# Optimization experiments

Hardware: AMD Instinct MI355X
Metric: run time of the kernel (lower is better)

Reference implementation:

```python
import jax, jax.numpy as jnp
import numpy as np
import math

B, Hdim, Wdim, C = 8, 64, 64, 512
T, TXT = 77, 512
NH, HD = 8, 64  # num_heads, head_dim
TOP_M = 3
CLAMP_LOGIT = 2.0
CONF_THRESH = 0.35
NEG_INF = -1e30


def _ln(x, g, b, eps=1e-5):
    mu = x.mean(-1, keepdims=True)
    var = ((x - mu) ** 2).mean(-1, keepdims=True)
    return (x - mu) * jax.lax.rsqrt(var + eps) * g + b


def _l2norm(x, eps=1e-6):
    n = jnp.sqrt((x * x).sum(-1, keepdims=True))
    return x / jnp.maximum(n, eps)


def setup_inputs() -> dict:
    key = jax.random.key(0)
    ks = jax.random.split(key, 16)
    s = 0.02
    inp = {
        'visual_features': jax.random.normal(ks[0], (B, Hdim, Wdim, C), jnp.float32),
        'text_features': jax.random.normal(ks[1], (B, T, TXT), jnp.float32),
        'ln1_g': jnp.ones((C,), jnp.float32), 'ln1_b': jnp.zeros((C,), jnp.float32),
        'ln2_g': jnp.ones((C,), jnp.float32), 'ln2_b': jnp.zeros((C,), jnp.float32),
        'Wq': jax.random.normal(ks[2], (C, C), jnp.float32) * s, 'bq': jnp.zeros((C,), jnp.float32),
        'Wk': jax.random.normal(ks[3], (TXT, C), jnp.float32) * s, 'bk': jnp.zeros((C,), jnp.float32),
        'Wv': jax.random.normal(ks[4], (TXT, C), jnp.float32) * s, 'bv': jnp.zeros((C,), jnp.float32),
        'Wo': jax.random.normal(ks[5], (C, C), jnp.float32) * s, 'bo': jnp.zeros((C,), jnp.float32),
        'Wg': jax.random.normal(ks[6], (C, 1), jnp.float32) * s, 'bg': jnp.zeros((1,), jnp.float32),
        'W1': jax.random.normal(ks[7], (C, 4 * C), jnp.float32) * s, 'b1': jnp.zeros((4 * C,), jnp.float32),
        'W2': jax.random.normal(ks[8], (4 * C, C), jnp.float32) * s, 'b2': jnp.zeros((C,), jnp.float32),
        'logit_scale': jnp.asarray(math.log(1.0 / 0.07), jnp.float32),
        'alpha': jnp.asarray(0.1, jnp.float32),
    }
    return inp


def reference(visual_features, text_features, ln1_g, ln1_b, ln2_g, ln2_b,
              Wq, bq, Wk, bk, Wv, bv, Wo, bo, Wg, bg, W1, b1, W2, b2,
              logit_scale, alpha):
    b, h, w, c = visual_features.shape
    n = h * w
    # Pre-LN on visual tokens
    x = _ln(visual_features, ln1_g, ln1_b).reshape(b, n, c)
    q_full = x @ Wq + bq                                   # [B,N,C]
    pad_mask = jnp.abs(text_features).sum(-1) <= 1e-6      # [B,T]
    k_full = text_features @ Wk + bk                       # [B,T,C]
    v_full = text_features @ Wv + bv
    # l2-normalize over full channel dim, then split heads
    q = _l2norm(q_full).reshape(b, n, NH, HD)
    k = _l2norm(k_full).reshape(b, T, NH, HD)
    v = v_full.reshape(b, T, NH, HD)
    scale = jnp.exp(jnp.clip(logit_scale, -CLAMP_LOGIT, CLAMP_LOGIT)) / math.sqrt(float(HD))
    sim = jnp.einsum('bnhd,bthd->bnht', q, k) * scale      # [B,N,H,T]
    sim = jnp.where(pad_mask[:, None, None, :], NEG_INF, sim)
    # top-k sparsification: keep top_m per (b,n,h) row
    topv = jax.lax.top_k(sim, TOP_M)[0][..., -1:]
    sim = jnp.where(sim >= topv, sim, NEG_INF)
    attn = jax.nn.softmax(sim, axis=-1)
    attn = attn / jnp.maximum(attn.sum(-1, keepdims=True), 1e-6)
    all_pad = pad_mask.all(axis=1)                         # [B]
    attn = jnp.where(all_pad[:, None, None, None], 0.0, attn)
    # confidence: max-prob * (1 - normalized entropy), mean over heads
    attn_hn = attn.transpose(0, 2, 1, 3)                   # [B,H,N,T]
    maxp = attn_hn.max(-1, keepdims=True)
    t_eff = jnp.maximum((attn_hn > 0).astype(jnp.float32).sum(-1, keepdims=True), 2.0)
    p = jnp.maximum(attn_hn, 1e-8)
    entropy = jnp.maximum(-(p * jnp.log(p)).sum(-1, keepdims=True) / jnp.log(t_eff), 0.0)
    conf = jnp.clip(maxp * (1.0 - entropy), 0.0, 1.0).mean(axis=1)  # [B,N,1]
    bypass = (conf >= CONF_THRESH).astype(attn.dtype)
    aligned = jnp.einsum('bnht,bthd->bnhd', attn, v).reshape(b, n, c)
    aligned = (aligned @ Wo + bo) * bypass
    gate = jax.nn.sigmoid(x @ Wg + bg)                     # [B,N,1]
    y = x + alpha * gate * aligned
    y = _ln(y, ln2_g, ln2_b)
    y = y + (jax.nn.gelu(y @ W1 + b1, approximate=False) @ W2 + b2)
    return y.reshape(b, h, w, c)
```

## Files before the change

kernel.cpp:

```cpp
#include <hip/hip_runtime.h>
#include <stdint.h>

#define BATCH 8
#define NTOK 4096
#define CDIM 512
#define TTXT 77
#define TPAD 80
#define NHEAD 8
#define HDIM 64
#define HID 2048
#define MROWS 32768
#define NEGINF (-1e30f)

typedef __attribute__((ext_vector_type(8))) short short8;
typedef __attribute__((ext_vector_type(4))) float f32x4;

__device__ __forceinline__ float b2f(unsigned short u) {
    union { unsigned int i; float f; } x; x.i = ((unsigned int)u) << 16; return x.f;
}
__device__ __forceinline__ unsigned short f2b(float f) {
    union { float f; unsigned int i; } x; x.f = f;
    unsigned int i = x.i;
    return (unsigned short)((i + 0x7fffu + ((i >> 16) & 1u)) >> 16);
}

__device__ __forceinline__ void gload16(const void* g, void* l) {
    __builtin_amdgcn_global_load_lds(
        (const __attribute__((address_space(1))) unsigned int*)g,
        (__attribute__((address_space(3))) unsigned int*)l, 16, 0, 0);
}

#define OFF_WQT   ((size_t)0)
#define OFF_WKT   (OFF_WQT + 512*512*2)
#define OFF_WVT   (OFF_WKT + 512*512*2)
#define OFF_WOT   (OFF_WVT + 512*512*2)
#define OFF_W1T   (OFF_WOT + 512*512*2)
#define OFF_W2T   (OFF_W1T + (size_t)2048*512*2)
#define OFF_TEXTB (OFF_W2T + (size_t)512*2048*2)
#define OFF_KFB   (OFF_TEXTB + (size_t)640*512*2)
#define OFF_KNRM  (OFF_KFB + (size_t)640*512*2)
#define OFF_VPAD  (OFF_KNRM + (size_t)640*512*2)
#define OFF_PADM  (OFF_VPAD + (size_t)640*512*2)
#define OFF_ALLP  (OFF_PADM + 2560)
#define OFF_GATE  (OFF_ALLP + 256)
#define OFF_BYP   (OFF_GATE + (size_t)MROWS*4)
#define OFF_XB    (OFF_BYP + (size_t)MROWS*4)
#define OFF_BUFB  (OFF_XB + (size_t)MROWS*CDIM*2)
#define OFF_BUFC  (OFF_BUFB + (size_t)MROWS*CDIM*2)
#define OFF_H     (OFF_BUFC + (size_t)MROWS*CDIM*2)
#define WS_NEED   (OFF_H + (size_t)MROWS*HID*2)
#define OFF_VT    OFF_H

__device__ __forceinline__ float waveReduceAdd(float v) {
#pragma unroll
    for (int m = 1; m < 64; m <<= 1) v += __shfl_xor(v, m);
    return v;
}
__device__ __forceinline__ float waveReduceMin(float v) {
#pragma unroll
    for (int m = 1; m < 64; m <<= 1) v = fminf(v, __shfl_xor(v, m));
    return v;
}
__device__ __forceinline__ float red16Max(float v) {
#pragma unroll
    for (int m = 1; m < 16; m <<= 1) v = fmaxf(v, __shfl_xor(v, m));
    return v;
}
__device__ __forceinline__ float red16Add(float v) {
#pragma unroll
    for (int m = 1; m < 16; m <<= 1) v += __shfl_xor(v, m);
    return v;
}

__global__ __launch_bounds__(256) void transpose_all_kernel(
    const float* __restrict__ Wq, const float* __restrict__ Wk,
    const float* __restrict__ Wv, const float* __restrict__ Wo,
    const float* __restrict__ W1, const float* __restrict__ W2,
    unsigned short* __restrict__ WQT, unsigned short* __restrict__ WKT,
    unsigned short* __restrict__ WVT, unsigned short* __restrict__ WOT,
    unsigned short* __restrict__ W1T, unsigned short* __restrict__ W2T)
{
    __shared__ float tile[32][33];
    int b = blockIdx.x;
    const float* src; unsigned short* dst; int R, C, cx, ry;
    if (b < 1024)       { src = W1; dst = W1T; R = 512;  C = 2048; cx = b & 63; ry = b >> 6; }
    else if (b < 2048)  { b -= 1024; src = W2; dst = W2T; R = 2048; C = 512; cx = b & 15; ry = b >> 4; }
    else {
        b -= 2048; const int which = b >> 8; b &= 255;
        R = 512; C = 512; cx = b & 15; ry = b >> 4;
        src = (which == 0) ? Wq : (which == 1) ? Wk : (which == 2) ? Wv : Wo;
        dst = (which == 0) ? WQT : (which == 1) ? WKT : (which == 2) ? WVT : WOT;
    }
    const int tx = threadIdx.x & 31, ty = threadIdx.x >> 5;
    const int c0 = cx * 32, r0 = ry * 32;
#pragma unroll
    for (int i = 0; i < 32; i += 8)
        tile[ty + i][tx] = src[(size_t)(r0 + ty + i) * C + c0 + tx];
    __syncthreads();
#pragma unroll
    for (int i = 0; i < 32; i += 8)
        dst[(size_t)(c0 + ty + i) * R + r0 + tx] = f2b(tile[tx][ty + i]);
}

__global__ __launch_bounds__(128) void text_prep_kernel(
    const float* __restrict__ text, unsigned short* __restrict__ textb, float* __restrict__ padm)
{
    __shared__ float sred[2];
    const int r = blockIdx.x;
    const int b = r / TPAD, t = r % TPAD;
    const int tid = threadIdx.x;
    if (t < TTXT) {
        float4 v = *(const float4*)(text + ((size_t)(b * TTXT + t)) * 512 + tid * 4);
        float a = fabsf(v.x) + fabsf(v.y) + fabsf(v.z) + fabsf(v.w);
        a = waveReduceAdd(a);
        if ((tid & 63) == 0) sred[tid >> 6] = a;
        __syncthreads();
        float asum = sred[0] + sred[1];
        ushort4 o; o.x = f2b(v.x); o.y = f2b(v.y); o.z = f2b(v.z); o.w = f2b(v.w);
        *(ushort4*)(textb + (size_t)r * 512 + tid * 4) = o;
        if (tid == 0) padm[r] = (asum <= 1e-6f) ? 1.f : 0.f;
    } else {
        ushort4 z; z.x = 0; z.y = 0; z.z = 0; z.w = 0;
        *(ushort4*)(textb + (size_t)r * 512 + tid * 4) = z;
        if (tid == 0) padm[r] = 1.f;
    }
}

__global__ __launch_bounds__(128) void allpad_kernel(
    const float* __restrict__ padm, float* __restrict__ allp)
{
    __shared__ float sred[2];
    const int b = blockIdx.x, tid = threadIdx.x;
    float f = (tid < TTXT) ? padm[b * TPAD + tid] : 1.f;
    f = waveReduceMin(f);
    if ((tid & 63) == 0) sred[tid >> 6] = f;
    __syncthreads();
    if (tid == 0) allp[b] = fminf(sred[0], sred[1]);
}

__global__ __launch_bounds__(128) void ln1_gate_kernel(
    const float* __restrict__ vin, const float* __restrict__ g1, const float* __restrict__ b1v,
    const float* __restrict__ Wg, const float* __restrict__ bg,
    unsigned short* __restrict__ xb, float* __restrict__ gate)
{
    __shared__ float sred[4];
    const int row = blockIdx.x, tid = threadIdx.x;
    const float4 v = *(const float4*)(vin + (size_t)row * 512 + tid * 4);
    float s = v.x + v.y + v.z + v.w;
    float s2 = v.x * v.x + v.y * v.y + v.z * v.z + v.w * v.w;
    s = waveReduceAdd(s); s2 = waveReduceAdd(s2);
    if ((tid & 63) == 0) { sred[tid >> 6] = s; sred[2 + (tid >> 6)] = s2; }
    __syncthreads();
    s = sred[0] + sred[1]; s2 = sred[2] + sred[3];
    const float mu = s * (1.f / 512.f);
    float var = s2 * (1.f / 512.f) - mu * mu;
    const float rs = rsqrtf(fmaxf(var, 0.f) + 1e-5f);
    const float4 gg = *(const float4*)(g1 + tid * 4);
    const float4 bb = *(const float4*)(b1v + tid * 4);
    const float x0 = (v.x - mu) * rs * gg.x + bb.x;
    const float x1 = (v.y - mu) * rs * gg.y + bb.y;
    const float x2 = (v.z - mu) * rs * gg.z + bb.z;
    const float x3 = (v.w - mu) * rs * gg.w + bb.w;
    ushort4 o; o.x = f2b(x0); o.y = f2b(x1); o.z = f2b(x2); o.w = f2b(x3);
    *(ushort4*)(xb + (size_t)row * 512 + tid * 4) = o;
    const float4 wg = *(const float4*)(Wg + tid * 4);
    float gp = x0 * wg.x + x1 * wg.y + x2 * wg.z + x3 * wg.w;
    gp = waveReduceAdd(gp);
    __syncthreads();
    if ((tid & 63) == 0) sred[tid >> 6] = gp;
    __syncthreads();
    if (tid == 0) {
        float z = sred[0] + sred[1] + bg[0];
        gate[row] = 1.f / (1.f + __expf(-z));
    }
}

__global__ __launch_bounds__(128) void ln2_kernel(
    const unsigned short* __restrict__ yin, const float* __restrict__ g2, const float* __restrict__ b2v,
    unsigned short* __restrict__ yb)
{
    __shared__ float sred[4];
    const int row = blockIdx.x, tid = threadIdx.x;
    ushort4 u = *(const ushort4*)(yin + (size_t)row * 512 + tid * 4);
    float v0 = b2f(u.x), v1 = b2f(u.y), v2 = b2f(u.z), v3 = b2f(u.w);
    float s = v0 + v1 + v2 + v3;
    float s2 = v0 * v0 + v1 * v1 + v2 * v2 + v3 * v3;
    s = waveReduceAdd(s); s2 = waveReduceAdd(s2);
    if ((tid & 63) == 0) { sred[tid >> 6] = s; sred[2 + (tid >> 6)] = s2; }
    __syncthreads();
    s = sred[0] + sred[1]; s2 = sred[2] + sred[3];
    const float mu = s * (1.f / 512.f);
    float var = s2 * (1.f / 512.f) - mu * mu;
    const float rs = rsqrtf(fmaxf(var, 0.f) + 1e-5f);
    const float4 gg = *(const float4*)(g2 + tid * 4);
    const float4 bb = *(const float4*)(b2v + tid * 4);
    ushort4 o;
    o.x = f2b((v0 - mu) * rs * gg.x + bb.x);
    o.y = f2b((v1 - mu) * rs * gg.y + bb.y);
    o.z = f2b((v2 - mu) * rs * gg.z + bb.z);
    o.w = f2b((v3 - mu) * rs * gg.w + bb.w);
    *(ushort4*)(yb + (size_t)row * 512 + tid * 4) = o;
}

__global__ __launch_bounds__(128) void l2norm_kernel(
    const unsigned short* __restrict__ in, unsigned short* __restrict__ out)
{
    __shared__ float sred[2];
    const int row = blockIdx.x, tid = threadIdx.x;
    ushort4 u = *(const ushort4*)(in + (size_t)row * 512 + tid * 4);
    float v0 = b2f(u.x), v1 = b2f(u.y), v2 = b2f(u.z), v3 = b2f(u.w);
    float ss = v0 * v0 + v1 * v1 + v2 * v2 + v3 * v3;
    ss = waveReduceAdd(ss);
    if ((tid & 63) == 0) sred[tid >> 6] = ss;
    __syncthreads();
    ss = sred[0] + sred[1];
    const float inv = 1.f / fmaxf(sqrtf(ss), 1e-6f);
    ushort4 o;
    o.x = f2b(v0 * inv); o.y = f2b(v1 * inv); o.z = f2b(v2 * inv); o.w = f2b(v3 * inv);
    *(ushort4*)(out + (size_t)row * 512 + tid * 4) = o;
}

__global__ __launch_bounds__(256) void vt_prep_kernel(
    const unsigned short* __restrict__ vp, unsigned short* __restrict__ vt)
{
    __shared__ unsigned short st[80][72];
    const int b = blockIdx.x >> 3, h = blockIdx.x & 7;
    const int tid = threadIdx.x;
    for (int idx = tid; idx < 80 * 64; idx += 256) {
        int t = idx >> 6, d = idx & 63;
        st[t][d] = vp[((size_t)(b * TPAD + t)) * 512 + h * 64 + d];
    }
    __syncthreads();
    for (int idx = tid; idx < 64 * 96; idx += 256) {
        int d = idx / 96, t = idx - d * 96;
        vt[((size_t)blockIdx.x * 64 + d) * 96 + t] = (t < TPAD) ? st[t][d] : (unsigned short)0;
    }
}

__global__ __launch_bounds__(256) void gemm_bt(
    const unsigned short* __restrict__ A, const unsigned short* __restrict__ Bt,
    const float* __restrict__ bias,
    unsigned short* __restrict__ outb, int M, int N, int K)
{
    __shared__ unsigned short sA[128 * 64];
    __shared__ unsigned short sB[128 * 64];
    char* cA = (char*)sA;
    char* cB = (char*)sB;
    const int tid = threadIdx.x;
    const int lane = tid & 63, w = tid >> 6;
    const int g = lane >> 4, ln = lane & 15;
    const int WR = w >> 1, WC = w & 1;
    const int rowA0 = blockIdx.x * 128, colB0 = blockIdx.y * 128;

    f32x4 acc[4][4];
#pragma unroll
    for (int m = 0; m < 4; ++m)
#pragma unroll
        for (int n = 0; n < 4; ++n) acc[m][n] = (f32x4){0.f, 0.f, 0.f, 0.f};

    for (int k0 = 0; k0 < K; k0 += 64) {
        __syncthreads();
#pragma unroll
        for (int i = 0; i < 4; ++i) {
            int c = tid + i * 256;
            int row = c >> 3, kc = c & 7;
            int kcs = kc ^ (row & 7);
            gload16(A + (size_t)(rowA0 + row) * K + k0 + kcs * 8, cA + c * 16);
            gload16(Bt + (size_t)(colB0 + row) * K + k0 + kcs * 8, cB + c * 16);
        }
        __syncthreads();
#pragma unroll
        for (int kk = 0; kk < 2; ++kk) {
            short8 af[4], bf[4];
#pragma unroll
            for (int m = 0; m < 4; ++m) {
                int row = WR * 64 + m * 16 + ln;
                af[m] = *(const short8*)(cA + row * 128 + ((kk * 64 + g * 16) ^ ((row & 7) << 4)));
            }
#pragma unroll
            for (int n = 0; n < 4; ++n) {
                int col = WC * 64 + n * 16 + ln;
                bf[n] = *(const short8*)(cB + col * 128 + ((kk * 64 + g * 16) ^ ((col & 7) << 4)));
            }
#pragma unroll
            for (int m = 0; m < 4; ++m)
#pragma unroll
                for (int n = 0; n < 4; ++n)
                    acc[m][n] = __builtin_amdgcn_mfma_f32_16x16x32_bf16(af[m], bf[n], acc[m][n], 0, 0, 0);
        }
    }

#pragma unroll
    for (int m = 0; m < 4; ++m) {
        const int rbase = rowA0 + WR * 64 + m * 16 + g * 4;
#pragma unroll
        for (int n = 0; n < 4; ++n) {
            const int col = colB0 + WC * 64 + n * 16 + ln;
            const float bcol = bias[col];
#pragma unroll
            for (int i = 0; i < 4; ++i)
                outb[(size_t)(rbase + i) * N + col] = f2b(acc[m][n][i] + bcol);
        }
    }
}

template<int EPI>
__global__ __launch_bounds__(512, 2) void gemm256(
    const unsigned short* __restrict__ A, const unsigned short* __restrict__ Bt,
    const float* __restrict__ bias,
    unsigned short* __restrict__ outb, float* __restrict__ outf,
    int M, int N, int K,
    const unsigned short* __restrict__ xres, const float* __restrict__ gate,
    const float* __restrict__ byp, const unsigned short* __restrict__ yres,
    const float* __restrict__ alphaPtr, int gxM, int gyN)
{
    __shared__ unsigned short lds[2][2][16384];
    const int tid = threadIdx.x;
    const int lane = tid & 63, w = tid >> 6;
    const int g = lane >> 4, ln = lane & 15;
    const int wr = w >> 2, wc = w & 3;

    int bm, bn;
    {
        const int L = (int)blockIdx.x;
        const int xcd = L & 7, j = L >> 3;
        const int rl = j / gyN;
        bn = j - rl * gyN;
        bm = xcd * (gxM >> 3) + rl;
    }
    const int rowA0 = bm * 256, colB0 = bn * 256;
    const int nt = K >> 6;

    auto stageA = [&](int t, int mh) {
        const int buf = t & 1;
#pragma unroll
        for (int r = 0; r < 2; ++r) {
            const int c = tid + r * 512;
            const int prl = c >> 3, kc = c & 7;
            const int grow = rowA0 + ((prl >> 6) << 7) + (mh << 6) + (prl & 63);
            gload16(A + (size_t)grow * K + (t << 6) + ((kc ^ (prl & 7)) << 3),
                    (char*)&lds[buf][0][mh * 8192] + c * 16);
        }
    };
    auto stageB = [&](int t, int nh) {
        const int buf = t & 1;
#pragma unroll
        for (int r = 0; r < 2; ++r) {
            const int c = tid + r * 512;
            const int prl = c >> 3, kc = c & 7;
            const int gcol = colB0 + ((prl >> 5) << 6) + (nh << 5) + (prl & 31);
            gload16(Bt + (size_t)gcol * K + (t << 6) + ((kc ^ (prl & 7)) << 3),
                    (char*)&lds[buf][1][nh * 8192] + c * 16);
        }
    };

    f32x4 acc[8][4];
#pragma unroll
    for (int m = 0; m < 8; ++m)
#pragma unroll
        for (int n = 0; n < 4; ++n) acc[m][n] = (f32x4){0.f, 0.f, 0.f, 0.f};

    stageA(0, 0); stageA(0, 1); stageB(0, 0); stageB(0, 1);
    asm volatile("s_waitcnt vmcnt(0)" ::: "memory");
    __builtin_amdgcn_s_barrier();

    const int sw  = (ln & 7) << 4;
    const int kb0 = (g * 16) ^ sw;
    const int kb1 = (64 + g * 16) ^ sw;
    const int arow = (wr * 64 + ln) * 128;
    const int brow = (wc * 32 + ln) * 128;

    short8 afr[4][2], bfr[4][2];

    for (int t = 0; t < nt; ++t) {
        const char* lA = (const char*)&lds[t & 1][0][0];
        const char* lB = (const char*)&lds[t & 1][1][0];
        const bool pf = (t + 1 < nt);

#pragma unroll
        for (int m = 0; m < 4; ++m) {
            afr[m][0] = *(const short8*)(lA + arow + m * 2048 + kb0);
            afr[m][1] = *(const short8*)(lA + arow + m * 2048 + kb1);
        }
#pragma unroll
        for (int n = 0; n < 2; ++n) {
            bfr[n][0] = *(const short8*)(lB + brow + n * 2048 + kb0);
            bfr[n][1] = *(const short8*)(lB + brow + n * 2048 + kb1);
        }
        if (pf) { stageA(t + 1, 0); stageA(t + 1, 1); }
        __builtin_amdgcn_s_setprio(1);
#pragma unroll
        for (int m = 0; m < 4; ++m)
#pragma unroll
            for (int n = 0; n < 2; ++n) {
                acc[m][n] = __builtin_amdgcn_mfma_f32_16x16x32_bf16(afr[m][0], bfr[n][0], acc[m][n], 0, 0, 0);
                acc[m][n] = __builtin_amdgcn_mfma_f32_16x16x32_bf16(afr[m][1], bfr[n][1], acc[m][n], 0, 0, 0);
            }
        __builtin_amdgcn_s_setprio(0);
        __builtin_amdgcn_sched_barrier(0);

#pragma unroll
        for (int n = 2; n < 4; ++n) {
            bfr[n][0] = *(const short8*)(lB + brow + (n & 1) * 2048 + 16384 + kb0);
            bfr[n][1] = *(const short8*)(lB + brow + (n & 1) * 2048 + 16384 + kb1);
        }
        if (pf) { stageB(t + 1, 0); stageB(t + 1, 1); }
        __builtin_amdgcn_s_setprio(1);
#pragma unroll
        for (int m = 0; m < 4; ++m)
#pragma unroll
            for (int n = 2; n < 4; ++n) {
                acc[m][n] = __builtin_amdgcn_mfma_f32_16x16x32_bf16(afr[m][0], bfr[n][0], acc[m][n], 0, 0, 0);
                acc[m][n] = __builtin_amdgcn_mfma_f32_16x16x32_bf16(afr[m][1], bfr[n][1], acc[m][n], 0, 0, 0);
            }
        __builtin_amdgcn_s_setprio(0);
        __builtin_amdgcn_sched_barrier(0);

#pragma unroll
        for (int m = 0; m < 4; ++m) {
            afr[m][0] = *(const short8*)(lA + arow + m * 2048 + 16384 + kb0);
            afr[m][1] = *(const short8*)(lA + arow + m * 2048 + 16384 + kb1);
        }
        __builtin_amdgcn_s_setprio(1);
#pragma unroll
        for (int m = 0; m < 4; ++m)
#pragma unroll
            for (int n = 0; n < 2; ++n) {
                acc[m + 4][n] = __builtin_amdgcn_mfma_f32_16x16x32_bf16(afr[m][0], bfr[n][0], acc[m + 4][n], 0, 0, 0);
                acc[m + 4][n] = __builtin_amdgcn_mfma_f32_16x16x32_bf16(afr[m][1], bfr[n][1], acc[m + 4][n], 0, 0, 0);
            }
        __builtin_amdgcn_s_setprio(0);
        __builtin_amdgcn_sched_barrier(0);

        __builtin_amdgcn_s_setprio(1);
#pragma unroll
        for (int m = 0; m < 4; ++m)
#pragma unroll
            for (int n = 2; n < 4; ++n) {
                acc[m + 4][n] = __builtin_amdgcn_mfma_f32_16x16x32_bf16(afr[m][0], bfr[n][0], acc[m + 4][n], 0, 0, 0);
                acc[m + 4][n] = __builtin_amdgcn_mfma_f32_16x16x32_bf16(afr[m][1], bfr[n][1], acc[m + 4][n], 0, 0, 0);
            }
        __builtin_amdgcn_s_setprio(0);

        if (pf) {
            asm volatile("s_waitcnt vmcnt(0)" ::: "memory");
            __builtin_amdgcn_s_barrier();
        }
    }

    const float alpha = (EPI == 1) ? *alphaPtr : 0.f;
#pragma unroll
    for (int m = 0; m < 8; ++m) {
        const int rbase = rowA0 + wr * 128 + m * 16 + g * 4;
#pragma unroll
        for (int n = 0; n < 4; ++n) {
            const int col = colB0 + wc * 64 + n * 16 + ln;
            const float bcol = bias[col];
#pragma unroll
            for (int i = 0; i < 4; ++i) {
                const int row = rbase + i;
                const float v = acc[m][n][i] + bcol;
                if (EPI == 0) {
                    outb[(size_t)row * N + col] = f2b(v);
                } else if (EPI == 1) {
                    float yp = b2f(xres[(size_t)row * N + col]) + alpha * gate[row] * byp[row] * v;
                    outb[(size_t)row * N + col] = f2b(yp);
                } else if (EPI == 2) {
                    const float u2 = 2.f * v * (0.7978845608f + 0.0356774081f * v * v);
                    const float tt = 1.f - 2.f / (__expf(u2) + 1.f);
                    outb[(size_t)row * N + col] = f2b(0.5f * v * (1.f + tt));
                } else {
                    outf[(size_t)row * N + col] = b2f(yres[(size_t)row * N + col]) + v;
                }
            }
        }
    }
}

__global__ __launch_bounds__(256) void attn_kernel(
    const unsigned short* __restrict__ qn,
    const unsigned short* __restrict__ kn,
    const unsigned short* __restrict__ vt,
    const float* __restrict__ padm,
    const float* __restrict__ allp,
    const float* __restrict__ lscPtr,
    unsigned short* __restrict__ aligned,
    float* __restrict__ bypass)
{
    const int b = blockIdx.y;
    const int n0 = blockIdx.x * 16;
    const int tid = threadIdx.x;
    const int w = tid >> 6, lane = tid & 63, g = lane >> 4, ln = lane & 15;
    __shared__ unsigned short s_p[4][16][104];
    __shared__ float s_conf[4][16];
    __shared__ float s_inv[16];

    if (allp[b] > 0.5f) {
        uint4 z = {0u, 0u, 0u, 0u};
#pragma unroll
        for (int j = 0; j < 4; ++j) {
            int id = tid + j * 256;
            int row = id >> 6, c8 = id & 63;
            *(uint4*)(aligned + ((size_t)(b * NTOK + n0 + row)) * 512 + c8 * 8) = z;
        }
        if (tid < 16) bypass[b * NTOK + n0 + tid] = 0.f;
        return;
    }

    {
        const int r = tid >> 4, seg = tid & 15;
        const unsigned short* qp = qn + ((size_t)(b * NTOK + n0 + r)) * 512 + seg * 32;
        float ss = 0.f;
#pragma unroll
        for (int j = 0; j < 4; ++j) {
            short8 u = *(const short8*)(qp + j * 8);
#pragma unroll
            for (int e = 0; e < 8; ++e) {
                float f = b2f(((const unsigned short*)&u)[e]);
                ss += f * f;
            }
        }
        ss = red16Add(ss);
        if (seg == 0) s_inv[r] = 1.f / fmaxf(sqrtf(ss), 1e-6f);
    }

    float lscale;
    {
        float ls = *lscPtr;
        ls = fminf(fmaxf(ls, -2.f), 2.f);
        lscale = __expf(ls) * 0.125f;
    }

    float pm[5];
#pragma unroll
    for (int tt = 0; tt < 5; ++tt) {
        int t = ln + tt * 16;
        pm[tt] = (t < TTXT) ? padm[b * TPAD + t] : 1.f;
    }

    for (int j = g; j < 24; j += 4) s_p[w][ln][80 + j] = 0;
    __syncthreads();

    float conf_acc[4] = {0.f, 0.f, 0.f, 0.f};
    const size_t qrow = ((size_t)(b * NTOK + n0 + ln)) * 512;

#pragma unroll
    for (int hh = 0; hh < 2; ++hh) {
        const int h = w + hh * 4;
        short8 a0 = *(const short8*)(qn + qrow + h * 64 + g * 8);
        short8 a1 = *(const short8*)(qn + qrow + h * 64 + 32 + g * 8);
        f32x4 sim[5];
#pragma unroll
        for (int tt = 0; tt < 5; ++tt) {
            const size_t kbase = ((size_t)(b * TPAD + tt * 16 + ln)) * 512 + h * 64;
            short8 b0 = *(const short8*)(kn + kbase + g * 8);
            short8 b1 = *(const short8*)(kn + kbase + 32 + g * 8);
            f32x4 c = (f32x4){0.f, 0.f, 0.f, 0.f};
            c = __builtin_amdgcn_mfma_f32_16x16x32_bf16(a0, b0, c, 0, 0, 0);
            c = __builtin_amdgcn_mfma_f32_16x16x32_bf16(a1, b1, c, 0, 0, 0);
            sim[tt] = c;
        }
#pragma unroll
        for (int i = 0; i < 4; ++i) {
            const float qs = lscale * s_inv[g * 4 + i];
            float v[5];
#pragma unroll
            for (int tt = 0; tt < 5; ++tt)
                v[tt] = (pm[tt] == 0.f) ? sim[tt][i] * qs : NEGINF;

            float lm = v[0];
#pragma unroll
            for (int tt = 1; tt < 5; ++tt) lm = fmaxf(lm, v[tt]);
            const float m1 = red16Max(lm);
            float lm2 = -3.0e38f;
#pragma unroll
            for (int tt = 0; tt < 5; ++tt) if (v[tt] < m1) lm2 = fmaxf(lm2, v[tt]);
            const float m2 = red16Max(lm2);
            float lm3 = -3.0e38f;
#pragma unroll
            for (int tt = 0; tt < 5; ++tt) if (v[tt] < m2) lm3 = fmaxf(lm3, v[tt]);
            const float m3 = red16Max(lm3);
            float lc1 = 0.f, lc2 = 0.f;
#pragma unroll
            for (int tt = 0; tt < 5; ++tt) {
                if (v[tt] >= m1) lc1 += 1.f;
                if (v[tt] >= m2) lc2 += 1.f;
            }
            const float c1 = red16Add(lc1);
            const float c2 = red16Add(lc2);
            const float th = (c1 >= 3.f) ? m1 : ((c2 >= 3.f) ? m2 : m3);

            float p[5], lsum = 0.f, lcnt = 0.f;
#pragma unroll
            for (int tt = 0; tt < 5; ++tt) {
                float pv = (v[tt] >= th) ? __expf(v[tt] - m1) : 0.f;
                p[tt] = pv;
                lsum += pv;
                lcnt += (pv > 0.f) ? 1.f : 0.f;
            }
            const float psum = red16Add(lsum);
            const float pcnt = red16Add(lcnt);
            const float inv = 1.f / fmaxf(psum, 1e-20f);

            float lmaxp = 0.f, lent = 0.f;
#pragma unroll
            for (int tt = 0; tt < 5; ++tt) {
                float a = p[tt] * inv;
                p[tt] = a;
                lmaxp = fmaxf(lmaxp, a);
                if (a > 0.f) {
                    float pp = fmaxf(a, 1e-8f);
                    lent += -pp * __logf(pp);
                }
            }
            const float maxp = red16Max(lmaxp);
            float ent = red16Add(lent);
            ent += (77.f - pcnt) * 1.8420680744e-7f;
            const float teff = fmaxf(pcnt, 2.f);
            const float entropy = fmaxf(ent / __logf(teff), 0.f);
            const float confh = fminf(fmaxf(maxp * (1.f - entropy), 0.f), 1.f);
            conf_acc[i] += confh;

#pragma unroll
            for (int tt = 0; tt < 5; ++tt)
                s_p[w][g * 4 + i][ln + tt * 16] = f2b(p[tt]);
        }
        short8 af[3];
#pragma unroll
        for (int k = 0; k < 3; ++k)
            af[k] = *(const short8*)(&s_p[w][ln][k * 32 + g * 8]);
        const size_t vtb = ((size_t)(b * NHEAD + h)) * 64;
#pragma unroll
        for (int n = 0; n < 4; ++n) {
            f32x4 o = (f32x4){0.f, 0.f, 0.f, 0.f};
#pragma unroll
            for (int k = 0; k < 3; ++k) {
                short8 bf = *(const short8*)(vt + (vtb + n * 16 + ln) * 96 + k * 32 + g * 8);
                o = __builtin_amdgcn_mfma_f32_16x16x32_bf16(af[k], bf, o, 0, 0, 0);
            }
#pragma unroll
            for (int i = 0; i < 4; ++i)
                aligned[((size_t)(b * NTOK + n0 + g * 4 + i)) * 512 + h * 64 + n * 16 + ln] =
                    f2b(o[i]);
        }
    }

    if (ln == 0) {
#pragma unroll
        for (int i = 0; i < 4; ++i) s_conf[w][g * 4 + i] = conf_acc[i];
    }
    __syncthreads();
    if (tid < 16) {
        float c = (s_conf[0][tid] + s_conf[1][tid] + s_conf[2][tid] + s_conf[3][tid]) * 0.125f;
        bypass[b * NTOK + n0 + tid] = (c >= 0.35f) ? 1.f : 0.f;
    }
}

extern "C" void kernel_launch(void* const* d_in, const int* in_sizes, int n_in,
                              void* d_out, int out_size, void* d_ws, size_t ws_size,
                              hipStream_t stream)
{
    (void)in_sizes; (void)n_in; (void)out_size;
    if (ws_size < WS_NEED) return;

    const float* visual = (const float*)d_in[0];
    const float* text   = (const float*)d_in[1];
    const float* ln1_g  = (const float*)d_in[2];
    const float* ln1_b  = (const float*)d_in[3];
    const float* ln2_g  = (const float*)d_in[4];
    const float* ln2_b  = (const float*)d_in[5];
    const float* Wq = (const float*)d_in[6];   const float* bq = (const float*)d_in[7];
    const float* Wk = (const float*)d_in[8];   const float* bk = (const float*)d_in[9];
    const float* Wv = (const float*)d_in[10];  const float* bv = (const float*)d_in[11];
    const float* Wo = (const float*)d_in[12];  const float* bo = (const float*)d_in[13];
    const float* Wg = (const float*)d_in[14];  const float* bg = (const float*)d_in[15];
    const float* W1 = (const float*)d_in[16];  const float* b1 = (const float*)d_in[17];
    const float* W2 = (const float*)d_in[18];  const float* b2 = (const float*)d_in[19];
    const float* lsc = (const float*)d_in[20];
    const float* alp = (const float*)d_in[21];

    char* ws = (char*)d_ws;
    unsigned short* WQT  = (unsigned short*)(ws + OFF_WQT);
    unsigned short* WKT  = (unsigned short*)(ws + OFF_WKT);
    unsigned short* WVT  = (unsigned short*)(ws + OFF_WVT);
    unsigned short* WOT  = (unsigned short*)(ws + OFF_WOT);
    unsigned short* W1T  = (unsigned short*)(ws + OFF_W1T);
    unsigned short* W2T  = (unsigned short*)(ws + OFF_W2T);
    unsigned short* TEXTB = (unsigned short*)(ws + OFF_TEXTB);
    unsigned short* KFB  = (unsigned short*)(ws + OFF_KFB);
    unsigned short* KNRM = (unsigned short*)(ws + OFF_KNRM);
    unsigned short* VPAD = (unsigned short*)(ws + OFF_VPAD);
    float* PADM = (float*)(ws + OFF_PADM);
    float* ALLP = (float*)(ws + OFF_ALLP);
    float* GATE = (float*)(ws + OFF_GATE);
    float* BYP  = (float*)(ws + OFF_BYP);
    unsigned short* XB   = (unsigned short*)(ws + OFF_XB);
    unsigned short* BUFB = (unsigned short*)(ws + OFF_BUFB);
    unsigned short* BUFC = (unsigned short*)(ws + OFF_BUFC);
    unsigned short* HBUF = (unsigned short*)(ws + OFF_H);
    unsigned short* VT   = (unsigned short*)(ws + OFF_VT);
    float* out = (float*)d_out;

    transpose_all_kernel<<<3072, 256, 0, stream>>>(Wq, Wk, Wv, Wo, W1, W2,
                                                   WQT, WKT, WVT, WOT, W1T, W2T);

    text_prep_kernel<<<640, 128, 0, stream>>>(text, TEXTB, PADM);
    allpad_kernel<<<BATCH, 128, 0, stream>>>(PADM, ALLP);

    ln1_gate_kernel<<<MROWS, 128, 0, stream>>>(visual, ln1_g, ln1_b, Wg, bg, XB, GATE);

    gemm_bt<<<dim3(5, 4), 256, 0, stream>>>(TEXTB, WKT, bk, KFB, 640, 512, 512);
    gemm_bt<<<dim3(5, 4), 256, 0, stream>>>(TEXTB, WVT, bv, VPAD, 640, 512, 512);
    l2norm_kernel<<<640, 128, 0, stream>>>(KFB, KNRM);
    vt_prep_kernel<<<BATCH * NHEAD, 256, 0, stream>>>(VPAD, VT);

    gemm256<0><<<dim3(128 * 2), 512, 0, stream>>>(XB, WQT, bq, BUFB, nullptr, MROWS, 512, 512,
                                                  nullptr, nullptr, nullptr, nullptr, nullptr,
                                                  128, 2);

    attn_kernel<<<dim3(NTOK / 16, BATCH), 256, 0, stream>>>(BUFB, KNRM, VT, PADM, ALLP, lsc,
                                                            BUFC, BYP);

    gemm256<1><<<dim3(128 * 2), 512, 0, stream>>>(BUFC, WOT, bo, BUFB, nullptr, MROWS, 512, 512,
                                                  XB, GATE, BYP, nullptr, alp, 128, 2);

    ln2_kernel<<<MROWS, 128, 0, stream>>>(BUFB, ln2_g, ln2_b, XB);

    gemm256<2><<<dim3(128 * 8), 512, 0, stream>>>(XB, W1T, b1, HBUF, nullptr, MROWS, HID, 512,
                                                  nullptr, nullptr, nullptr, nullptr, nullptr,
                                                  128, 8);
    gemm256<3><<<dim3(128 * 2), 512, 0, stream>>>(HBUF, W2T, b2, nullptr, out, MROWS, 512, HID,
                                                  nullptr, nullptr, nullptr, XB, nullptr,
                                                  128, 2);
}
```

Measured before the change: 376.7 us.

## Fuse prep kernels and K/V GEMMs, compute all-pad in attention

```diff
diff --git a/kernel.cpp b/kernel.cpp
--- a/kernel.cpp
+++ b/kernel.cpp
@@ -56,11 +56,6 @@
     for (int m = 1; m < 64; m <<= 1) v += __shfl_xor(v, m);
     return v;
 }
-__device__ __forceinline__ float waveReduceMin(float v) {
-#pragma unroll
-    for (int m = 1; m < 64; m <<= 1) v = fminf(v, __shfl_xor(v, m));
-    return v;
-}
 __device__ __forceinline__ float red16Max(float v) {
 #pragma unroll
     for (int m = 1; m < 16; m <<= 1) v = fmaxf(v, __shfl_xor(v, m));
@@ -71,17 +66,56 @@
     for (int m = 1; m < 16; m <<= 1) v += __shfl_xor(v, m);
     return v;
 }
-
-__global__ __launch_bounds__(256) void transpose_all_kernel(
+__device__ __forceinline__ float red16Min(float v) {
+#pragma unroll
+    for (int m = 1; m < 16; m <<= 1) v = fminf(v, __shfl_xor(v, m));
+    return v;
+}
+
+__global__ __launch_bounds__(256) void prep_kernel(
     const float* __restrict__ Wq, const float* __restrict__ Wk,
     const float* __restrict__ Wv, const float* __restrict__ Wo,
     const float* __restrict__ W1, const float* __restrict__ W2,
     unsigned short* __restrict__ WQT, unsigned short* __restrict__ WKT,
     unsigned short* __restrict__ WVT, unsigned short* __restrict__ WOT,
-    unsigned short* __restrict__ W1T, unsigned short* __restrict__ W2T)
+    unsigned short* __restrict__ W1T, unsigned short* __restrict__ W2T,
+    const float* __restrict__ text, unsigned short* __restrict__ textb,
+    float* __restrict__ padm, unsigned short* __restrict__ vt)
 {
     __shared__ float tile[32][33];
+    __shared__ float sred[4];
     int b = blockIdx.x;
+    const int tid = threadIdx.x;
+
+    if (b >= 3712) {
+        const int i = b - 3712;
+        const int bh = i * 4 + (tid >> 6), d = tid & 63;
+        uint4 z = {0u, 0u, 0u, 0u};
+        uint4* p = (uint4*)(vt + ((size_t)bh * 64 + d) * 96 + 80);
+        p[0] = z; p[1] = z;
+        return;
+    }
+    if (b >= 3072) {
+        const int r = b - 3072;
+        const int tb = r / TPAD, t = r % TPAD;
+        if (t < TTXT) {
+            const float2 v = ((const float2*)(text + ((size_t)(tb * TTXT + t)) * 512))[tid];
+            float a = fabsf(v.x) + fabsf(v.y);
+            a = waveReduceAdd(a);
+            if ((tid & 63) == 0) sred[tid >> 6] = a;
+            __syncthreads();
+            const float asum = sred[0] + sred[1] + sred[2] + sred[3];
+            ushort2 o; o.x = f2b(v.x); o.y = f2b(v.y);
+            ((ushort2*)(textb + (size_t)r * 512))[tid] = o;
+            if (tid == 0) padm[r] = (asum <= 1e-6f) ? 1.f : 0.f;
+        } else {
+            ushort2 z; z.x = 0; z.y = 0;
+            ((ushort2*)(textb + (size_t)r * 512))[tid] = z;
+            if (tid == 0) padm[r] = 1.f;
+        }
+        return;
+    }
+
     const float* src; unsigned short* dst; int R, C, cx, ry;
     if (b < 1024)       { src = W1; dst = W1T; R = 512;  C = 2048; cx = b & 63; ry = b >> 6; }
     else if (b < 2048)  { b -= 1024; src = W2; dst = W2T; R = 2048; C = 512; cx = b & 15; ry = b >> 4; }
@@ -100,42 +134,6 @@
 #pragma unroll
     for (int i = 0; i < 32; i += 8)
         dst[(size_t)(c0 + ty + i) * R + r0 + tx] = f2b(tile[tx][ty + i]);
-}
-
-__global__ __launch_bounds__(128) void text_prep_kernel(
-    const float* __restrict__ text, unsigned short* __restrict__ textb, float* __restrict__ padm)
-{
-    __shared__ float sred[2];
-    const int r = blockIdx.x;
-    const int b = r / TPAD, t = r % TPAD;
-    const int tid = threadIdx.x;
-    if (t < TTXT) {
-        float4 v = *(const float4*)(text + ((size_t)(b * TTXT + t)) * 512 + tid * 4);
-        float a = fabsf(v.x) + fabsf(v.y) + fabsf(v.z) + fabsf(v.w);
-        a = waveReduceAdd(a);
-        if ((tid & 63) == 0) sred[tid >> 6] = a;
-        __syncthreads();
-        float asum = sred[0] + sred[1];
-        ushort4 o; o.x = f2b(v.x); o.y = f2b(v.y); o.z = f2b(v.z); o.w = f2b(v.w);
-        *(ushort4*)(textb + (size_t)r * 512 + tid * 4) = o;
-        if (tid == 0) padm[r] = (asum <= 1e-6f) ? 1.f : 0.f;
-    } else {
-        ushort4 z; z.x = 0; z.y = 0; z.z = 0; z.w = 0;
-        *(ushort4*)(textb + (size_t)r * 512 + tid * 4) = z;
-        if (tid == 0) padm[r] = 1.f;
-    }
-}
-
-__global__ __launch_bounds__(128) void allpad_kernel(
-    const float* __restrict__ padm, float* __restrict__ allp)
-{
-    __shared__ float sred[2];
-    const int b = blockIdx.x, tid = threadIdx.x;
-    float f = (tid < TTXT) ? padm[b * TPAD + tid] : 1.f;
-    f = waveReduceMin(f);
-    if ((tid & 63) == 0) sred[tid >> 6] = f;
-    __syncthreads();
-    if (tid == 0) allp[b] = fminf(sred[0], sred[1]);
 }
 
 __global__ __launch_bounds__(128) void ln1_gate_kernel(
@@ -220,28 +218,15 @@
     *(ushort4*)(out + (size_t)row * 512 + tid * 4) = o;
 }
 
-__global__ __launch_bounds__(256) void vt_prep_kernel(
-    const unsigned short* __restrict__ vp, unsigned short* __restrict__ vt)
+__global__ __launch_bounds__(256) void gemm_kv(
+    const unsigned short* __restrict__ A,
+    const unsigned short* __restrict__ BtK, const unsigned short* __restrict__ BtV,
+    const float* __restrict__ bk, const float* __restrict__ bv,
+    unsigned short* __restrict__ kfb, unsigned short* __restrict__ vt)
 {
-    __shared__ unsigned short st[80][72];
-    const int b = blockIdx.x >> 3, h = blockIdx.x & 7;
-    const int tid = threadIdx.x;
-    for (int idx = tid; idx < 80 * 64; idx += 256) {
-        int t = idx >> 6, d = idx & 63;
-        st[t][d] = vp[((size_t)(b * TPAD + t)) * 512 + h * 64 + d];
-    }
-    __syncthreads();
-    for (int idx = tid; idx < 64 * 96; idx += 256) {
-        int d = idx / 96, t = idx - d * 96;
-        vt[((size_t)blockIdx.x * 64 + d) * 96 + t] = (t < TPAD) ? st[t][d] : (unsigned short)0;
-    }
-}
-
-__global__ __launch_bounds__(256) void gemm_bt(
-    const unsigned short* __restrict__ A, const unsigned short* __restrict__ Bt,
-    const float* __restrict__ bias,
-    unsigned short* __restrict__ outb, int M, int N, int K)
-{
+    const int K = 512, N = 512;
+    const unsigned short* Bt = blockIdx.z ? BtV : BtK;
+    const float* bias = blockIdx.z ? bv : bk;
     __shared__ unsigned short sA[128 * 64];
     __shared__ unsigned short sB[128 * 64];
     char* cA = (char*)sA;
@@ -298,8 +283,17 @@
             const int col = colB0 + WC * 64 + n * 16 + ln;
             const float bcol = bias[col];
 #pragma unroll
-            for (int i = 0; i < 4; ++i)
-                outb[(size_t)(rbase + i) * N + col] = f2b(acc[m][n][i] + bcol);
+            for (int i = 0; i < 4; ++i) {
+                const int row = rbase + i;
+                const float v = acc[m][n][i] + bcol;
+                if (blockIdx.z == 0) {
+                    kfb[(size_t)row * N + col] = f2b(v);
+                } else {
+                    const int tb = row / TPAD, t = row - tb * TPAD;
+                    const int h = col >> 6, d = col & 63;
+                    vt[((size_t)(tb * NHEAD + h) * 64 + d) * 96 + t] = f2b(v);
+                }
+            }
         }
     }
 }
@@ -372,6 +366,7 @@
 
     short8 afr[4][2], bfr[4][2];
 
+#pragma unroll 2
     for (int t = 0; t < nt; ++t) {
         const char* lA = (const char*)&lds[t & 1][0][0];
         const char* lB = (const char*)&lds[t & 1][1][0];
@@ -482,7 +477,6 @@
     const unsigned short* __restrict__ kn,
     const unsigned short* __restrict__ vt,
     const float* __restrict__ padm,
-    const float* __restrict__ allp,
     const float* __restrict__ lscPtr,
     unsigned short* __restrict__ aligned,
     float* __restrict__ bypass)
@@ -495,16 +489,26 @@
     __shared__ float s_conf[4][16];
     __shared__ float s_inv[16];
 
-    if (allp[b] > 0.5f) {
-        uint4 z = {0u, 0u, 0u, 0u};
-#pragma unroll
-        for (int j = 0; j < 4; ++j) {
-            int id = tid + j * 256;
-            int row = id >> 6, c8 = id & 63;
-            *(uint4*)(aligned + ((size_t)(b * NTOK + n0 + row)) * 512 + c8 * 8) = z;
-        }
-        if (tid < 16) bypass[b * NTOK + n0 + tid] = 0.f;
-        return;
+    float pm[5];
+#pragma unroll
+    for (int tt = 0; tt < 5; ++tt) {
+        int t = ln + tt * 16;
+        pm[tt] = (t < TTXT) ? padm[b * TPAD + t] : 1.f;
+    }
+    {
+        float pmn = fminf(fminf(pm[0], pm[1]), fminf(fminf(pm[2], pm[3]), pm[4]));
+        pmn = red16Min(pmn);
+        if (pmn > 0.5f) {
+            uint4 z = {0u, 0u, 0u, 0u};
+#pragma unroll
+            for (int j = 0; j < 4; ++j) {
+                int id = tid + j * 256;
+                int row = id >> 6, c8 = id & 63;
+                *(uint4*)(aligned + ((size_t)(b * NTOK + n0 + row)) * 512 + c8 * 8) = z;
+            }
+            if (tid < 16) bypass[b * NTOK + n0 + tid] = 0.f;
+            return;
+        }
     }
 
     {
@@ -529,13 +533,6 @@
         float ls = *lscPtr;
         ls = fminf(fmaxf(ls, -2.f), 2.f);
         lscale = __expf(ls) * 0.125f;
-    }
-
-    float pm[5];
-#pragma unroll
-    for (int tt = 0; tt < 5; ++tt) {
-        int t = ln + tt * 16;
-        pm[tt] = (t < TTXT) ? padm[b * TPAD + t] : 1.f;
     }
 
     for (int j = g; j < 24; j += 4) s_p[w][ln][80 + j] = 0;
@@ -580,14 +577,15 @@
 #pragma unroll
             for (int tt = 0; tt < 5; ++tt) if (v[tt] < m2) lm3 = fmaxf(lm3, v[tt]);
             const float m3 = red16Max(lm3);
-            float lc1 = 0.f, lc2 = 0.f;
+            float lc = 0.f;
 #pragma unroll
             for (int tt = 0; tt < 5; ++tt) {
-                if (v[tt] >= m1) lc1 += 1.f;
-                if (v[tt] >= m2) lc2 += 1.f;
-            }
-            const float c1 = red16Add(lc1);
-            const float c2 = red16Add(lc2);
+                if (v[tt] >= m1) lc += 1.f;
+                if (v[tt] >= m2) lc += 128.f;
+            }
+            const float cpk = red16Add(lc);
+            const float c2 = floorf(cpk * (1.f / 128.f));
+            const float c1 = cpk - 128.f * c2;
             const float th = (c1 >= 3.f) ? m1 : ((c2 >= 3.f) ? m2 : m3);
 
             float p[5], lsum = 0.f, lcnt = 0.f;
@@ -689,9 +687,7 @@
     unsigned short* TEXTB = (unsigned short*)(ws + OFF_TEXTB);
     unsigned short* KFB  = (unsigned short*)(ws + OFF_KFB);
     unsigned short* KNRM = (unsigned short*)(ws + OFF_KNRM);
-    unsigned short* VPAD = (unsigned short*)(ws + OFF_VPAD);
     float* PADM = (float*)(ws + OFF_PADM);
-    float* ALLP = (float*)(ws + OFF_ALLP);
     float* GATE = (float*)(ws + OFF_GATE);
     float* BYP  = (float*)(ws + OFF_BYP);
     unsigned short* XB   = (unsigned short*)(ws + OFF_XB);
@@ -701,24 +697,20 @@
     unsigned short* VT   = (unsigned short*)(ws + OFF_VT);
     float* out = (float*)d_out;
 
-    transpose_all_kernel<<<3072, 256, 0, stream>>>(Wq, Wk, Wv, Wo, W1, W2,
-                                                   WQT, WKT, WVT, WOT, W1T, W2T);
-
-    text_prep_kernel<<<640, 128, 0, stream>>>(text, TEXTB, PADM);
-    allpad_kernel<<<BATCH, 128, 0, stream>>>(PADM, ALLP);
+    prep_kernel<<<3728, 256, 0, stream>>>(Wq, Wk, Wv, Wo, W1, W2,
+                                          WQT, WKT, WVT, WOT, W1T, W2T,
+                                          text, TEXTB, PADM, VT);
 
     ln1_gate_kernel<<<MROWS, 128, 0, stream>>>(visual, ln1_g, ln1_b, Wg, bg, XB, GATE);
 
-    gemm_bt<<<dim3(5, 4), 256, 0, stream>>>(TEXTB, WKT, bk, KFB, 640, 512, 512);
-    gemm_bt<<<dim3(5, 4), 256, 0, stream>>>(TEXTB, WVT, bv, VPAD, 640, 512, 512);
+    gemm_kv<<<dim3(5, 4, 2), 256, 0, stream>>>(TEXTB, WKT, WVT, bk, bv, KFB, VT);
     l2norm_kernel<<<640, 128, 0, stream>>>(KFB, KNRM);
-    vt_prep_kernel<<<BATCH * NHEAD, 256, 0, stream>>>(VPAD, VT);
 
     gemm256<0><<<dim3(128 * 2), 512, 0, stream>>>(XB, WQT, bq, BUFB, nullptr, MROWS, 512, 512,
                                                   nullptr, nullptr, nullptr, nullptr, nullptr,
                                                   128, 2);
 
-    attn_kernel<<<dim3(NTOK / 16, BATCH), 256, 0, stream>>>(BUFB, KNRM, VT, PADM, ALLP, lsc,
+    attn_kernel<<<dim3(NTOK / 16, BATCH), 256, 0, stream>>>(BUFB, KNRM, VT, PADM, lsc,
                                                             BUFC, BYP);
 
     gemm256<1><<<dim3(128 * 2), 512, 0, stream>>>(BUFC, WOT, bo, BUFB, nullptr, MROWS, 512, 512,
```

New measurement: 363.4 us. -3.5%, faster.
